# Performance work log

Hardware: AMD Instinct MI355X
Metric: run time of the kernel (lower is better)

The kernel has to match this reference:

```python
import jax, jax.numpy as jnp
import numpy as np

HEADS = 8
DIM_HEAD = 64
DIM_INNER = HEADS * DIM_HEAD  # 512
LLM_EMB = 4096
OUT_DIM = 512
ROPE_BASE = 10000.0
EPS = 1e-6


def rms_norm(x, w):
    # GemmaRMSNorm: normalize in fp32, scale by (1 + weight)
    x32 = x.astype(jnp.float32)
    var = jnp.mean(x32 * x32, axis=-1, keepdims=True)
    out = x32 * jax.lax.rsqrt(var + EPS)
    return (out * (1.0 + w)).astype(x.dtype)


def rope(x, offset):
    # x: [b, h, n, d]; half-split (LLaMA-style) rotary embedding
    d = x.shape[-1]
    n = x.shape[-2]
    inv_freq = 1.0 / (ROPE_BASE ** (jnp.arange(0, d, 2, dtype=jnp.float32) / d))
    pos = jnp.arange(n, dtype=jnp.float32) + offset
    freqs = pos[:, None] * inv_freq[None, :]          # [n, d/2]
    cos = jnp.concatenate([jnp.cos(freqs), jnp.cos(freqs)], axis=-1)  # [n, d]
    sin = jnp.concatenate([jnp.sin(freqs), jnp.sin(freqs)], axis=-1)
    x1, x2 = x[..., : d // 2], x[..., d // 2 :]
    rot = jnp.concatenate([-x2, x1], axis=-1)
    return x * cos + rot * sin


def setup_inputs() -> dict:
    key = jax.random.key(0)
    ks = jax.random.split(key, 20)
    b, n_plan, s_vlm = 4, 1024, 512
    s = 0.02
    return {
        "planning_tokens": jax.random.normal(ks[0], (b, n_plan, DIM_INNER), jnp.float32),
        "vlm_keys": jax.random.normal(ks[1], (b, s_vlm, LLM_EMB), jnp.float32),
        "vlm_values": jax.random.normal(ks[2], (b, s_vlm, LLM_EMB), jnp.float32),
        "W_skv": jax.random.normal(ks[3], (LLM_EMB, DIM_INNER), jnp.float32) * s,
        "b_skv": jnp.zeros((DIM_INNER,), jnp.float32),
        "W_qkv": jax.random.normal(ks[4], (DIM_INNER, 3 * DIM_INNER), jnp.float32) * s,
        "b_qkv": jnp.zeros((3 * DIM_INNER,), jnp.float32),
        "W_out": jax.random.normal(ks[5], (DIM_INNER, DIM_INNER), jnp.float32) * s,
        "b_out": jnp.zeros((DIM_INNER,), jnp.float32),
        "W_ff1": jax.random.normal(ks[6], (DIM_INNER, DIM_INNER), jnp.float32) * s,
        "b_ff1": jnp.zeros((DIM_INNER,), jnp.float32),
        "W_ff2": jax.random.normal(ks[7], (DIM_INNER, OUT_DIM), jnp.float32) * s,
        "b_ff2": jnp.zeros((OUT_DIM,), jnp.float32),
        "g_norm1": jnp.zeros((DIM_INNER,), jnp.float32),
        "g_norm2": jnp.zeros((DIM_INNER,), jnp.float32),
    }


def reference(planning_tokens, vlm_keys, vlm_values, W_skv, b_skv, W_qkv, b_qkv,
              W_out, b_out, W_ff1, b_ff1, W_ff2, b_ff2, g_norm1, g_norm2):
    b, n, _ = planning_tokens.shape
    scale = DIM_HEAD ** -0.5

    normed = rms_norm(planning_tokens, g_norm1)
    qkv = normed @ W_qkv + b_qkv                       # [b, n, 3*dim_inner]
    q, k, v = jnp.split(qkv, 3, axis=-1)
    to_heads = lambda t: t.reshape(b, n, HEADS, DIM_HEAD).transpose(0, 2, 1, 3)
    q, k, v = to_heads(q), to_heads(k), to_heads(v)    # [b, h, n, d]

    # no KV cache: q_len == k_len, offsets 0
    q = rope(q, 0)
    k = rope(k, 0)

    state_kv = jnp.concatenate([vlm_keys, vlm_values], axis=1) @ W_skv + b_skv
    state_len = vlm_keys.shape[1]
    sk, sv = state_kv[:, :state_len], state_kv[:, state_len:]
    sh = lambda t: t.reshape(b, state_len, HEADS, DIM_HEAD).transpose(0, 2, 1, 3)
    sk, sv = sh(sk), sh(sv)                            # [b, h, s, d]

    keys = jnp.concatenate([sk, k], axis=2)            # [b, h, s+n, d]
    values = jnp.concatenate([sv, v], axis=2)

    sim = jnp.einsum('bhid,bhjd->bhij', q, keys) * scale  # [b, h, n, s+n]
    k_len = keys.shape[2]
    # tril(ones(n, k_len), diagonal=state_len): j <= i + state_len
    mask = jnp.arange(k_len)[None, :] <= (jnp.arange(n)[:, None] + state_len)
    sim = jnp.where(mask[None, None], sim, -jnp.inf)
    attn = jax.nn.softmax(sim, axis=-1)

    out = jnp.einsum('bhij,bhjd->bhid', attn, values)  # [b, h, n, d]
    out = out.transpose(0, 2, 1, 3).reshape(b, n, DIM_INNER)
    out = out @ W_out + b_out
    all_out = planning_tokens + out

    ffn = rms_norm(all_out, g_norm2) @ W_ff1 + b_ff1
    ffn = jax.nn.gelu(ffn, approximate=False) @ W_ff2 + b_ff2
    return all_out + ffn
```

## Files before the change

kernel.cpp:

```cpp
#include <hip/hip_runtime.h>
#include <math.h>

typedef unsigned short u16;
typedef unsigned short u16x8 __attribute__((ext_vector_type(8)));
typedef __bf16 bf16v8 __attribute__((ext_vector_type(8)));
typedef float f32x4 __attribute__((ext_vector_type(4)));

static __device__ __forceinline__ float b2f(u16 u){ union{unsigned v; float f;} x; x.v=((unsigned)u)<<16; return x.f; }
static __device__ __forceinline__ u16 f2b(float f){ union{float f; unsigned v;} x; x.f=f; unsigned r=x.v+0x7fffu+((x.v>>16)&1u); return (u16)(r>>16); }
static __device__ __forceinline__ f32x4 mfma16(bf16v8 a, bf16v8 b, f32x4 c){
  return __builtin_amdgcn_mfma_f32_16x16x32_bf16(a,b,c,0,0,0);
}
#define GLDS16(g,l) __builtin_amdgcn_global_load_lds((const __attribute__((address_space(1))) unsigned*)(g), (__attribute__((address_space(3))) unsigned*)(l), 16, 0, 0)

__global__ __launch_bounds__(256) void prep_k(
    const float* __restrict__ vk, const float* __restrict__ vv, u16* __restrict__ vkc, u16* __restrict__ vvc,
    const float* __restrict__ Wqkv, const float* __restrict__ Wskv, const float* __restrict__ Wout,
    const float* __restrict__ Wff1, const float* __restrict__ Wff2,
    u16* __restrict__ Tqkv, u16* __restrict__ Tskv, u16* __restrict__ Tout,
    u16* __restrict__ Tff1, u16* __restrict__ Tff2,
    const float* __restrict__ x, const float* __restrict__ g, u16* __restrict__ o){
  __shared__ u16 tile[64][66];
  int blk = blockIdx.x, t = threadIdx.x;
  if (blk < 8192){
    int i = blk*256 + t;
    const float* s; u16* d; int j;
    if (i < 1048576){ s=vk; d=vkc; j=i; } else { s=vv; d=vvc; j=i-1048576; }
    const float* sp = s + (size_t)j*8;
    f32x4 a = *(const f32x4*)sp, b = *(const f32x4*)(sp+4);
    u16x8 ov;
    #pragma unroll
    for (int k=0;k<4;++k){ ov[k]=f2b(a[k]); ov[k+4]=f2b(b[k]); }
    *(u16x8*)(d + (size_t)j*8) = ov;
    return;
  }
  if (blk < 9088){
    int b2 = blk - 8192;
    const float* in; u16* out; int R, C, lb;
    if (b2 < 192){ in=Wqkv; out=Tqkv; R=512;  C=1536; lb=b2; }
    else if (b2 < 704){ in=Wskv; out=Tskv; R=4096; C=512; lb=b2-192; }
    else if (b2 < 768){ in=Wout; out=Tout; R=512; C=512; lb=b2-704; }
    else if (b2 < 832){ in=Wff1; out=Tff1; R=512; C=512; lb=b2-768; }
    else { in=Wff2; out=Tff2; R=512; C=512; lb=b2-832; }
    int ct = C >> 6;
    int bx = lb % ct, by = lb / ct;
    #pragma unroll
    for (int it=0; it<16; ++it){
      int idx = it*256 + t; int r = idx>>6, c = idx&63;
      tile[r][c] = f2b(in[(size_t)(by*64+r)*C + bx*64 + c]);
    }
    __syncthreads();
    #pragma unroll
    for (int it=0; it<16; ++it){
      int idx = it*256 + t; int c = idx>>6, r = idx&63;
      out[(size_t)(bx*64+c)*R + by*64 + r] = tile[r][c];
    }
    return;
  }
  int w = t>>6, l = t&63;
  size_t row = (size_t)(blk-9088)*4 + w;
  const float* xr = x + row*512 + l*8;
  f32x4 a = *(const f32x4*)xr, b = *(const f32x4*)(xr+4);
  float f[8]; float ss = 0.f;
  #pragma unroll
  for (int j=0;j<4;++j){ f[j]=a[j]; f[j+4]=b[j]; }
  #pragma unroll
  for (int j=0;j<8;++j) ss += f[j]*f[j];
  #pragma unroll
  for (int m=1;m<64;m<<=1) ss += __shfl_xor(ss, m, 64);
  float inv = rsqrtf(ss*(1.0f/512.f) + 1e-6f);
  f32x4 ga = *(const f32x4*)(g + l*8), gb = *(const f32x4*)(g + l*8 + 4);
  u16x8 ov;
  #pragma unroll
  for (int j=0;j<4;++j){ ov[j] = f2b(f[j]*inv*(1.f + ga[j])); ov[j+4] = f2b(f[j+4]*inv*(1.f + gb[j])); }
  *(u16x8*)(o + row*512 + l*8) = ov;
}

__global__ __launch_bounds__(256) void rmsn_k(const float* __restrict__ x, const float* __restrict__ g, u16* __restrict__ o){
  int w = threadIdx.x>>6, l = threadIdx.x&63;
  size_t row = (size_t)blockIdx.x*4 + w;
  const float* xr = x + row*512 + l*8;
  f32x4 a = *(const f32x4*)xr, b = *(const f32x4*)(xr+4);
  float f[8]; float ss = 0.f;
  #pragma unroll
  for (int j=0;j<4;++j){ f[j]=a[j]; f[j+4]=b[j]; }
  #pragma unroll
  for (int j=0;j<8;++j) ss += f[j]*f[j];
  #pragma unroll
  for (int m=1;m<64;m<<=1) ss += __shfl_xor(ss, m, 64);
  float inv = rsqrtf(ss*(1.0f/512.f) + 1e-6f);
  f32x4 ga = *(const f32x4*)(g + l*8), gb = *(const f32x4*)(g + l*8 + 4);
  u16x8 ov;
  #pragma unroll
  for (int j=0;j<4;++j){ ov[j] = f2b(f[j]*inv*(1.f + ga[j])); ov[j+4] = f2b(f[j+4]*inv*(1.f + gb[j])); }
  *(u16x8*)(o + row*512 + l*8) = ov;
}

template<int BM, int BN, int EPI, bool CONCAT, int SPLITS>
__global__ __launch_bounds__(256,2) void gemm_k(
  const u16* __restrict__ A, const u16* __restrict__ Avk, const u16* __restrict__ Avv,
  const u16* __restrict__ BT, const float* __restrict__ bias,
  u16* __restrict__ Cb, float* __restrict__ Cf,
  const float* __restrict__ resid, const float* __restrict__ addf,
  int M, int N, int K)
{
  constexpr int BK = 64;
  constexpr int MFR = BM/32, NFR = BN/32;
  __shared__ alignas(16) u16 sm[(BM+BN)*BK];
  u16* As = sm; u16* Bs = sm + BM*BK;
  const int t = threadIdx.x, w = t>>6, l = t&63, grp = l>>4, l16 = l&15;
  const int wr = w>>1, wc = w&1;
  const int m0 = blockIdx.x*BM, n0 = blockIdx.y*BN;
  const int kchunk = K/SPLITS, kbeg = blockIdx.z*kchunk, kend = kbeg + kchunk;

  f32x4 acc[MFR][NFR];
  #pragma unroll
  for (int m=0;m<MFR;++m)
    #pragma unroll
    for (int n=0;n<NFR;++n) acc[m][n] = f32x4{0.f,0.f,0.f,0.f};

  for (int k0 = kbeg; k0 < kend; k0 += BK){
    #pragma unroll
    for (int it=0; it<MFR; ++it){
      int p16 = it*256 + t;
      int row = p16>>3; int offb = (p16&7)<<4;
      int swz = offb ^ ((row&7)<<4);
      const u16* src;
      if (CONCAT){
        int g = m0+row, bb = g>>10, ii = g&1023;
        const u16* base = (ii < 512) ? (Avk + (size_t)(bb*512+ii)*4096)
                                     : (Avv + (size_t)(bb*512+ii-512)*4096);
        src = base + k0 + (swz>>1);
      } else {
        src = A + (size_t)(m0+row)*K + k0 + (swz>>1);
      }
      GLDS16(src, As + (it*256 + w*64)*8);
    }
    #pragma unroll
    for (int it=0; it<NFR; ++it){
      int p16 = it*256 + t;
      int row = p16>>3; int offb = (p16&7)<<4;
      int swz = offb ^ ((row&7)<<4);
      const u16* src = BT + (size_t)(n0+row)*K + k0 + (swz>>1);
      GLDS16(src, Bs + (it*256 + w*64)*8);
    }
    __syncthreads();

    bf16v8 af[MFR][2], bfr[NFR][2];
    #pragma unroll
    for (int kk=0;kk<2;++kk){
      #pragma unroll
      for (int m=0;m<MFR;++m){
        int row = wr*(BM/2) + m*16 + l16;
        int offb = (kk*64 + grp*16) ^ ((row&7)<<4);
        af[m][kk] = *(const bf16v8*)((const char*)As + row*128 + offb);
      }
      #pragma unroll
      for (int n=0;n<NFR;++n){
        int row = wc*(BN/2) + n*16 + l16;
        int offb = (kk*64 + grp*16) ^ ((row&7)<<4);
        bfr[n][kk] = *(const bf16v8*)((const char*)Bs + row*128 + offb);
      }
    }
    #pragma unroll
    for (int kk=0;kk<2;++kk)
      #pragma unroll
      for (int m=0;m<MFR;++m)
        #pragma unroll
        for (int n=0;n<NFR;++n)
          acc[m][n] = mfma16(af[m][kk], bfr[n][kk], acc[m][n]);
    __syncthreads();
  }

  #pragma unroll
  for (int m=0;m<MFR;++m){
    #pragma unroll
    for (int n=0;n<NFR;++n){
      #pragma unroll
      for (int r=0;r<4;++r){
        int row = m0 + wr*(BM/2) + m*16 + grp*4 + r;
        int col = n0 + wc*(BN/2) + n*16 + l16;
        size_t idx = (size_t)row*N + col;
        if (SPLITS > 1){
          Cf[(size_t)blockIdx.z*M*N + idx] = acc[m][n][r];
        } else {
          float v = acc[m][n][r] + bias[col];
          if (EPI == 0){
            Cb[idx] = f2b(v);
          } else if (EPI == 1){
            Cf[idx] = v + resid[idx];
          } else if (EPI == 2){
            v = 0.5f*v*(1.f + erff(v*0.70710678f));
            Cb[idx] = f2b(v);
          } else {
            Cf[idx] = v + addf[idx];
          }
        }
      }
    }
  }
}

template<int SPLITS>
__global__ __launch_bounds__(256) void combine_k(const float* __restrict__ P, const float* __restrict__ bias,
                                                 u16* __restrict__ outb, int n8, int N){
  int i = blockIdx.x*256 + threadIdx.x;
  if (i >= n8) return;
  size_t base = (size_t)i*8;
  const size_t MN = (size_t)n8*8;
  float acc[8];
  {
    f32x4 a = *(const f32x4*)(P + base), b = *(const f32x4*)(P + base + 4);
    #pragma unroll
    for (int j=0;j<4;++j){ acc[j]=a[j]; acc[j+4]=b[j]; }
  }
  #pragma unroll
  for (int s=1;s<SPLITS;++s){
    f32x4 a = *(const f32x4*)(P + s*MN + base), b = *(const f32x4*)(P + s*MN + base + 4);
    #pragma unroll
    for (int j=0;j<4;++j){ acc[j]+=a[j]; acc[j+4]+=b[j]; }
  }
  int col0 = (int)(base % N);
  u16x8 o;
  #pragma unroll
  for (int j=0;j<8;++j) o[j] = f2b(acc[j] + bias[col0+j]);
  *(u16x8*)(outb + base) = o;
}

__global__ __launch_bounds__(256) void scatter_qk(const u16* __restrict__ qkv, const u16* __restrict__ skv,
                                                  u16* __restrict__ Qh, u16* __restrict__ KEYS){
  int bi = blockIdx.x;
  int b = bi>>10, i = bi&1023;
  int t = threadIdx.x;
  int h = t>>5, dp = t&31;
  const u16* qrow = qkv + (size_t)bi*1536;
  float invf = __expf(-(float)dp * (9.2103403720f/32.f));
  float fr = (float)i * invf;
  float sn, cs; __sincosf(fr, &sn, &cs);
  int bh = b*8 + h;
  float x1 = b2f(qrow[h*64+dp]), x2 = b2f(qrow[h*64+dp+32]);
  u16* qd = Qh + ((size_t)bh*1024 + i)*64;
  qd[dp]    = f2b((x1*cs - x2*sn)*0.125f);
  qd[dp+32] = f2b((x2*cs + x1*sn)*0.125f);
  x1 = b2f(qrow[512+h*64+dp]); x2 = b2f(qrow[512+h*64+dp+32]);
  u16* kd = KEYS + ((size_t)bh*1536 + 512 + i)*64;
  kd[dp]    = f2b(x1*cs - x2*sn);
  kd[dp+32] = f2b(x2*cs + x1*sn);
  if (i < 512){
    const u16* skrow = skv + ((size_t)b*1024 + i)*512;
    for (int e = t; e < 512; e += 256){
      int hh = e>>6, d = e&63;
      KEYS[((size_t)(b*8+hh)*1536 + i)*64 + d] = skrow[e];
    }
  }
}

__global__ __launch_bounds__(256) void build_vt(const u16* __restrict__ qkv, const u16* __restrict__ skv,
                                                u16* __restrict__ VT){
  __shared__ u16 tile[64][66];
  int blk = blockIdx.x;
  int bh = blk / 24, tt = blk % 24;
  int b = bh>>3, h = bh&7;
  int t = threadIdx.x;
  int jbase;
  if (tt < 16){
    int i0 = tt*64; jbase = 512 + i0;
    #pragma unroll
    for (int it=0; it<16; ++it){
      int idx = it*256+t; int r = idx>>6, c = idx&63;
      tile[r][c] = qkv[((size_t)b*1024 + i0 + r)*1536 + 1024 + h*64 + c];
    }
  } else {
    int j0 = (tt-16)*64; jbase = j0;
    #pragma unroll
    for (int it=0; it<16; ++it){
      int idx = it*256+t; int r = idx>>6, c = idx&63;
      tile[r][c] = skv[((size_t)b*1024 + 512 + j0 + r)*512 + h*64 + c];
    }
  }
  __syncthreads();
  #pragma unroll
  for (int it=0; it<16; ++it){
    int idx = it*256+t; int c = idx>>6, r = idx&63;
    VT[((size_t)bh*64 + c)*1536 + jbase + r] = tile[r][c];
  }
}

__global__ __launch_bounds__(256,2) void attn_k(const u16* __restrict__ Qh, const u16* __restrict__ KEYS,
                                                const u16* __restrict__ VT,
                                                float* __restrict__ Op, float2* __restrict__ Ml2){
  __shared__ alignas(16) u16 Ks[2][64*64];
  __shared__ alignas(16) u16 Vs[2][64*64];
  __shared__ alignas(16) u16 Pl[4][2][16*64];
  const int t = threadIdx.x, w = t>>6, l = t&63, grp = l>>4, l16 = l&15;
  const int blk = blockIdx.x;
  const int s = blk & 1, qg = (blk>>1) & 7, bh = blk>>4;
  const int i0 = qg*128 + w*32;
  const int klo = s*768;
  int khi = qg*128 + 640; { int cap = klo + 768; if (khi > cap) khi = cap; }
  const size_t prow = ((size_t)s*32 + bh)*1024;

  if (khi <= klo){
    if (l < 32) Ml2[prow + i0 + l] = make_float2(-1e30f, 0.f);
    return;
  }
  const int nt = (khi - klo) >> 6;

  const u16* Qb = Qh + (size_t)bh*65536;
  const u16* Kb = KEYS + (size_t)bh*98304;
  const u16* Vb = VT + (size_t)bh*98304;
  const int swz = (l16&7)<<4;

  bf16v8 qf[2][2];
  #pragma unroll
  for (int m=0;m<2;++m)
    #pragma unroll
    for (int kk=0;kk<2;++kk)
      qf[m][kk] = *(const bf16v8*)(Qb + (size_t)(i0 + m*16 + l16)*64 + kk*32 + grp*8);

  f32x4 Ot[2][4];
  #pragma unroll
  for (int m=0;m<2;++m)
    #pragma unroll
    for (int n=0;n<4;++n) Ot[m][n] = f32x4{0.f,0.f,0.f,0.f};
  float mrun[2] = {-1e30f,-1e30f}, lrun[2] = {0.f,0.f};

  #pragma unroll
  for (int it=0; it<2; ++it){
    int p16 = it*256 + t; int row = p16>>3; int sb = ((p16&7)<<4) ^ ((row&7)<<4);
    GLDS16(Kb + (size_t)(klo+row)*64 + (sb>>1), &Ks[0][0] + (it*256 + w*64)*8);
    GLDS16(Vb + (size_t)row*1536 + klo + (sb>>1), &Vs[0][0] + (it*256 + w*64)*8);
  }
  __syncthreads();

  for (int tt = 0; tt < nt; ++tt){
    const int j0 = klo + tt*64;
    if (tt+1 < nt){
      const int j1 = j0 + 64, c1 = (tt+1)&1;
      #pragma unroll
      for (int it=0; it<2; ++it){
        int p16 = it*256 + t; int row = p16>>3; int sb = ((p16&7)<<4) ^ ((row&7)<<4);
        GLDS16(Kb + (size_t)(j1+row)*64 + (sb>>1), &Ks[c1][0] + (it*256 + w*64)*8);
        GLDS16(Vb + (size_t)row*1536 + j1 + (sb>>1), &Vs[c1][0] + (it*256 + w*64)*8);
      }
    }
    const int c = tt&1;
    const char* Kt = (const char*)&Ks[c][0];
    const char* Vt = (const char*)&Vs[c][0];

    f32x4 St[2][4];
    #pragma unroll
    for (int m=0;m<2;++m)
      #pragma unroll
      for (int n=0;n<4;++n) St[m][n] = f32x4{0.f,0.f,0.f,0.f};
    #pragma unroll
    for (int kk=0;kk<2;++kk)
      #pragma unroll
      for (int n=0;n<4;++n){
        int row = n*16 + l16;
        bf16v8 kf = *(const bf16v8*)(Kt + row*128 + ((kk*64 + grp*16) ^ swz));
        St[0][n] = mfma16(kf, qf[0][kk], St[0][n]);
        St[1][n] = mfma16(kf, qf[1][kk], St[1][n]);
      }

    #pragma unroll
    for (int m=0;m<2;++m){
      const int qb = i0 + m*16;
      const bool tail = (j0 + 63 > qb + 512);
      const int qlim = qb + l16 + 512;
      float sv[4][4]; float m_loc = -1e30f;
      #pragma unroll
      for (int n=0;n<4;++n)
        #pragma unroll
        for (int r=0;r<4;++r){
          float x = St[m][n][r];
          if (tail && (j0 + n*16 + grp*4 + r > qlim)) x = -1e30f;
          sv[n][r] = x; m_loc = fmaxf(m_loc, x);
        }
      m_loc = fmaxf(m_loc, __shfl_xor(m_loc, 16, 64));
      m_loc = fmaxf(m_loc, __shfl_xor(m_loc, 32, 64));
      float mnew = fmaxf(mrun[m], m_loc);
      float alpha = __expf(mrun[m] - mnew);
      float rs = 0.f;
      unsigned pk[8];
      #pragma unroll
      for (int n=0;n<4;++n)
        #pragma unroll
        for (int c2=0;c2<2;++c2){
          float p0 = __expf(sv[n][2*c2]   - mnew);
          float p1 = __expf(sv[n][2*c2+1] - mnew);
          rs += p0 + p1;
          pk[n*2+c2] = (unsigned)f2b(p0) | ((unsigned)f2b(p1) << 16);
        }
      rs += __shfl_xor(rs, 16, 64);
      rs += __shfl_xor(rs, 32, 64);
      lrun[m] = lrun[m]*alpha + rs;
      mrun[m] = mnew;
      #pragma unroll
      for (int n=0;n<4;++n)
        #pragma unroll
        for (int r=0;r<4;++r) Ot[m][n][r] *= alpha;
      u16* Pw = &Pl[w][m][0];
      #pragma unroll
      for (int n=0;n<4;++n)
        #pragma unroll
        for (int c2=0;c2<2;++c2)
          *(unsigned*)((char*)Pw + l16*128 + ((n*32 + grp*8 + c2*4) ^ swz)) = pk[n*2+c2];
    }

    bf16v8 pb[2][2];
    #pragma unroll
    for (int m=0;m<2;++m){
      const char* Pw = (const char*)&Pl[w][m][0];
      pb[m][0] = *(const bf16v8*)(Pw + l16*128 + ((grp*16)      ^ swz));
      pb[m][1] = *(const bf16v8*)(Pw + l16*128 + ((64 + grp*16) ^ swz));
    }
    #pragma unroll
    for (int n=0;n<4;++n){
      int row = n*16 + l16;
      bf16v8 vf0 = *(const bf16v8*)(Vt + row*128 + ((grp*16)      ^ swz));
      bf16v8 vf1 = *(const bf16v8*)(Vt + row*128 + ((64 + grp*16) ^ swz));
      #pragma unroll
      for (int m=0;m<2;++m){
        Ot[m][n] = mfma16(vf0, pb[m][0], Ot[m][n]);
        Ot[m][n] = mfma16(vf1, pb[m][1], Ot[m][n]);
      }
    }
    __syncthreads();
  }

  #pragma unroll
  for (int m=0;m<2;++m){
    float* Tw = (float*)&Pl[w][m][0];
    #pragma unroll
    for (int hf=0; hf<2; ++hf){
      #pragma unroll
      for (int nn=0; nn<2; ++nn)
        #pragma unroll
        for (int r=0; r<4; ++r)
          *(float*)((char*)Tw + l16*128 + ((((nn*16 + grp*4 + r)*4)) ^ swz)) = Ot[m][hf*2+nn][r];
      f32x4 v0 = *(const f32x4*)((const char*)Tw + l16*128 + ((grp*32)      ^ swz));
      f32x4 v1 = *(const f32x4*)((const char*)Tw + l16*128 + ((grp*32 + 16) ^ swz));
      float* dst = Op + (prow + i0 + m*16 + l16)*64 + hf*32 + grp*8;
      *(f32x4*)dst = v0;
      *(f32x4*)(dst+4) = v1;
    }
  }
  if (grp == 0){
    #pragma unroll
    for (int m=0;m<2;++m)
      Ml2[prow + i0 + m*16 + l16] = make_float2(mrun[m], lrun[m]);
  }
}

__global__ __launch_bounds__(512) void attn_combine(const float* __restrict__ Op, const float2* __restrict__ Ml2,
                                                    u16* __restrict__ AO){
  int bi = blockIdx.x;
  int b = bi>>10, i = bi&1023;
  int t = threadIdx.x; int h = t>>6, d = t&63;
  int bh = b*8 + h;
  float2 ml0 = Ml2[(size_t)bh*1024 + i];
  float2 ml1 = Ml2[((size_t)32 + bh)*1024 + i];
  float M = fmaxf(ml0.x, ml1.x);
  float a0 = (ml0.y > 0.f) ? __expf(ml0.x - M) : 0.f;
  float a1 = (ml1.y > 0.f) ? __expf(ml1.x - M) : 0.f;
  float denom = a0*ml0.y + a1*ml1.y;
  float o = 0.f;
  if (a0 > 0.f) o += a0 * Op[((size_t)bh*1024 + i)*64 + d];
  if (a1 > 0.f) o += a1 * Op[(((size_t)32 + bh)*1024 + i)*64 + d];
  AO[((size_t)b*1024 + i)*512 + h*64 + d] = f2b(o / denom);
}

extern "C" void kernel_launch(void* const* d_in, const int* in_sizes, int n_in,
                              void* d_out, int out_size, void* d_ws, size_t ws_size,
                              hipStream_t stream) {
  const float* planning = (const float*)d_in[0];
  const float* vk   = (const float*)d_in[1];
  const float* vv   = (const float*)d_in[2];
  const float* Wskv = (const float*)d_in[3];
  const float* bskv = (const float*)d_in[4];
  const float* Wqkv = (const float*)d_in[5];
  const float* bqkv = (const float*)d_in[6];
  const float* Wout = (const float*)d_in[7];
  const float* bout = (const float*)d_in[8];
  const float* Wff1 = (const float*)d_in[9];
  const float* bff1 = (const float*)d_in[10];
  const float* Wff2 = (const float*)d_in[11];
  const float* bff2 = (const float*)d_in[12];
  const float* g1   = (const float*)d_in[13];
  const float* g2   = (const float*)d_in[14];
  float* outp = (float*)d_out;

  char* w8 = (char*)d_ws;
  size_t off = 0;
  auto take = [&](size_t n)->char*{ char* p = w8 + off; off += (n + 255) & ~(size_t)255; return p; };
  u16* vkc     = (u16*)take((size_t)4*512*4096*2);
  u16* vvc     = (u16*)take((size_t)4*512*4096*2);
  u16* WTqkv   = (u16*)take((size_t)1536*512*2);
  u16* WTskv   = (u16*)take((size_t)512*4096*2);
  u16* WTout   = (u16*)take((size_t)512*512*2);
  u16* WTff1   = (u16*)take((size_t)512*512*2);
  u16* WTff2   = (u16*)take((size_t)512*512*2);
  u16* normed1 = (u16*)take((size_t)4096*512*2);
  u16* qkv     = (u16*)take((size_t)4096*1536*2);
  u16* skv     = (u16*)take((size_t)4096*512*2);
  u16* Qh      = (u16*)take((size_t)32*1024*64*2);
  u16* KEYS    = (u16*)take((size_t)32*1536*64*2);
  u16* VT      = (u16*)take((size_t)32*64*1536*2);
  u16* AO      = (u16*)take((size_t)4096*512*2);
  float* all_out = (float*)take((size_t)4096*512*4);
  u16* normed2 = (u16*)take((size_t)4096*512*2);
  u16* h1      = (u16*)take((size_t)4096*512*2);
  float* Op    = (float*)take((size_t)2*32*1024*64*4);
  float2* Ml2  = (float2*)take((size_t)2*32*1024*8);
  float* Pd    = (float*)take((size_t)4*4096*512*4);
  (void)in_sizes; (void)n_in; (void)out_size; (void)ws_size;

  prep_k<<<dim3(10112), 256, 0, stream>>>(vk, vv, vkc, vvc,
                                          Wqkv, Wskv, Wout, Wff1, Wff2,
                                          WTqkv, WTskv, WTout, WTff1, WTff2,
                                          planning, g1, normed1);

  gemm_k<64,128,0,false,1><<<dim3(64,12), 256, 0, stream>>>(normed1,nullptr,nullptr, WTqkv, bqkv, qkv, nullptr, nullptr, nullptr, 4096, 1536, 512);
  gemm_k<128,64,0,true, 4><<<dim3(32,8,4), 256, 0, stream>>>(nullptr, vkc, vvc,     WTskv, bskv, nullptr, Pd, nullptr, nullptr, 4096, 512, 4096);
  combine_k<4><<<dim3(1024), 256, 0, stream>>>(Pd, bskv, skv, 262144, 512);

  scatter_qk<<<dim3(4096), 256, 0, stream>>>(qkv, skv, Qh, KEYS);
  build_vt<<<dim3(768), 256, 0, stream>>>(qkv, skv, VT);

  attn_k<<<dim3(512), 256, 0, stream>>>(Qh, KEYS, VT, Op, Ml2);
  attn_combine<<<dim3(4096), 512, 0, stream>>>(Op, Ml2, AO);

  gemm_k<64,64,1,false,1><<<dim3(64,8), 256, 0, stream>>>(AO, nullptr,nullptr, WTout, bout, nullptr, all_out, planning, nullptr, 4096, 512, 512);
  rmsn_k<<<dim3(1024), 256, 0, stream>>>(all_out, g2, normed2);
  gemm_k<64,64,2,false,1><<<dim3(64,8), 256, 0, stream>>>(normed2, nullptr,nullptr, WTff1, bff1, h1, nullptr, nullptr, nullptr, 4096, 512, 512);
  gemm_k<64,64,3,false,1><<<dim3(64,8), 256, 0, stream>>>(h1, nullptr,nullptr, WTff2, bff2, nullptr, outp, nullptr, all_out, 4096, 512, 512);
}
```

Measured before the change: 154.6 us.

## Interleave key tiles across split-K halves and shrink attention query tile

The attention kernel now gives each block 64 query rows (16 per wave) instead of 128, and launches twice as many blocks. Each block works on one of two interleaved halves of the key tiles (even or odd 64-column tiles) rather than a contiguous range. This balances causal-masked work evenly between the two splits and removes the blocks that previously had no work. The cost is that each loaded K/V tile now feeds only 16 query rows per wave, so operand reuse is halved and total K/V traffic goes up.

```diff
diff --git a/kernel.cpp b/kernel.cpp
--- a/kernel.cpp
+++ b/kernel.cpp
@@ -291,166 +291,133 @@
                                                 float* __restrict__ Op, float2* __restrict__ Ml2){
   __shared__ alignas(16) u16 Ks[2][64*64];
   __shared__ alignas(16) u16 Vs[2][64*64];
-  __shared__ alignas(16) u16 Pl[4][2][16*64];
+  __shared__ alignas(16) u16 Pl[4][16*64];
   const int t = threadIdx.x, w = t>>6, l = t&63, grp = l>>4, l16 = l&15;
   const int blk = blockIdx.x;
-  const int s = blk & 1, qg = (blk>>1) & 7, bh = blk>>4;
-  const int i0 = qg*128 + w*32;
-  const int klo = s*768;
-  int khi = qg*128 + 640; { int cap = klo + 768; if (khi > cap) khi = cap; }
+  const int s = blk & 1, qg = (blk>>1) & 15, bh = blk>>5;
+  const int i0 = qg*64 + w*16;
+  int khi = qg*64 + 576; if (khi > 1536) khi = 1536;
+  const int ntt = khi >> 6;
   const size_t prow = ((size_t)s*32 + bh)*1024;
-
-  if (khi <= klo){
-    if (l < 32) Ml2[prow + i0 + l] = make_float2(-1e30f, 0.f);
-    return;
-  }
-  const int nt = (khi - klo) >> 6;
 
   const u16* Qb = Qh + (size_t)bh*65536;
   const u16* Kb = KEYS + (size_t)bh*98304;
   const u16* Vb = VT + (size_t)bh*98304;
+  u16* Pw = &Pl[w][0];
   const int swz = (l16&7)<<4;
-
-  bf16v8 qf[2][2];
-  #pragma unroll
-  for (int m=0;m<2;++m)
-    #pragma unroll
-    for (int kk=0;kk<2;++kk)
-      qf[m][kk] = *(const bf16v8*)(Qb + (size_t)(i0 + m*16 + l16)*64 + kk*32 + grp*8);
-
-  f32x4 Ot[2][4];
-  #pragma unroll
-  for (int m=0;m<2;++m)
-    #pragma unroll
-    for (int n=0;n<4;++n) Ot[m][n] = f32x4{0.f,0.f,0.f,0.f};
-  float mrun[2] = {-1e30f,-1e30f}, lrun[2] = {0.f,0.f};
+  const int qlim = i0 + l16 + 512;
+
+  bf16v8 qf[2];
+  #pragma unroll
+  for (int kk=0;kk<2;++kk)
+    qf[kk] = *(const bf16v8*)(Qb + (size_t)(i0 + l16)*64 + kk*32 + grp*8);
+
+  f32x4 Ot[4];
+  #pragma unroll
+  for (int n=0;n<4;++n) Ot[n] = f32x4{0.f,0.f,0.f,0.f};
+  float mrun = -1e30f, lrun = 0.f;
 
   #pragma unroll
   for (int it=0; it<2; ++it){
     int p16 = it*256 + t; int row = p16>>3; int sb = ((p16&7)<<4) ^ ((row&7)<<4);
-    GLDS16(Kb + (size_t)(klo+row)*64 + (sb>>1), &Ks[0][0] + (it*256 + w*64)*8);
-    GLDS16(Vb + (size_t)row*1536 + klo + (sb>>1), &Vs[0][0] + (it*256 + w*64)*8);
+    GLDS16(Kb + (size_t)(s*64+row)*64 + (sb>>1), &Ks[0][0] + (it*256 + w*64)*8);
+    GLDS16(Vb + (size_t)row*1536 + s*64 + (sb>>1), &Vs[0][0] + (it*256 + w*64)*8);
   }
   __syncthreads();
 
-  for (int tt = 0; tt < nt; ++tt){
-    const int j0 = klo + tt*64;
-    if (tt+1 < nt){
-      const int j1 = j0 + 64, c1 = (tt+1)&1;
+  int buf = 0;
+  for (int tt = s; tt < ntt; tt += 2){
+    const int j0 = tt*64;
+    if (tt+2 < ntt){
+      const int j1 = j0 + 128, nb = buf^1;
       #pragma unroll
       for (int it=0; it<2; ++it){
         int p16 = it*256 + t; int row = p16>>3; int sb = ((p16&7)<<4) ^ ((row&7)<<4);
-        GLDS16(Kb + (size_t)(j1+row)*64 + (sb>>1), &Ks[c1][0] + (it*256 + w*64)*8);
-        GLDS16(Vb + (size_t)row*1536 + j1 + (sb>>1), &Vs[c1][0] + (it*256 + w*64)*8);
-      }
-    }
-    const int c = tt&1;
-    const char* Kt = (const char*)&Ks[c][0];
-    const char* Vt = (const char*)&Vs[c][0];
-
-    f32x4 St[2][4];
-    #pragma unroll
-    for (int m=0;m<2;++m)
-      #pragma unroll
-      for (int n=0;n<4;++n) St[m][n] = f32x4{0.f,0.f,0.f,0.f};
+        GLDS16(Kb + (size_t)(j1+row)*64 + (sb>>1), &Ks[nb][0] + (it*256 + w*64)*8);
+        GLDS16(Vb + (size_t)row*1536 + j1 + (sb>>1), &Vs[nb][0] + (it*256 + w*64)*8);
+      }
+    }
+    const char* Kt = (const char*)&Ks[buf][0];
+    const char* Vt = (const char*)&Vs[buf][0];
+
+    f32x4 St[4];
+    #pragma unroll
+    for (int n=0;n<4;++n) St[n] = f32x4{0.f,0.f,0.f,0.f};
     #pragma unroll
     for (int kk=0;kk<2;++kk)
       #pragma unroll
       for (int n=0;n<4;++n){
         int row = n*16 + l16;
         bf16v8 kf = *(const bf16v8*)(Kt + row*128 + ((kk*64 + grp*16) ^ swz));
-        St[0][n] = mfma16(kf, qf[0][kk], St[0][n]);
-        St[1][n] = mfma16(kf, qf[1][kk], St[1][n]);
-      }
-
-    #pragma unroll
-    for (int m=0;m<2;++m){
-      const int qb = i0 + m*16;
-      const bool tail = (j0 + 63 > qb + 512);
-      const int qlim = qb + l16 + 512;
-      float sv[4][4]; float m_loc = -1e30f;
-      #pragma unroll
-      for (int n=0;n<4;++n)
-        #pragma unroll
-        for (int r=0;r<4;++r){
-          float x = St[m][n][r];
-          if (tail && (j0 + n*16 + grp*4 + r > qlim)) x = -1e30f;
-          sv[n][r] = x; m_loc = fmaxf(m_loc, x);
-        }
-      m_loc = fmaxf(m_loc, __shfl_xor(m_loc, 16, 64));
-      m_loc = fmaxf(m_loc, __shfl_xor(m_loc, 32, 64));
-      float mnew = fmaxf(mrun[m], m_loc);
-      float alpha = __expf(mrun[m] - mnew);
-      float rs = 0.f;
-      unsigned pk[8];
-      #pragma unroll
-      for (int n=0;n<4;++n)
-        #pragma unroll
-        for (int c2=0;c2<2;++c2){
-          float p0 = __expf(sv[n][2*c2]   - mnew);
-          float p1 = __expf(sv[n][2*c2+1] - mnew);
-          rs += p0 + p1;
-          pk[n*2+c2] = (unsigned)f2b(p0) | ((unsigned)f2b(p1) << 16);
-        }
-      rs += __shfl_xor(rs, 16, 64);
-      rs += __shfl_xor(rs, 32, 64);
-      lrun[m] = lrun[m]*alpha + rs;
-      mrun[m] = mnew;
-      #pragma unroll
-      for (int n=0;n<4;++n)
-        #pragma unroll
-        for (int r=0;r<4;++r) Ot[m][n][r] *= alpha;
-      u16* Pw = &Pl[w][m][0];
-      #pragma unroll
-      for (int n=0;n<4;++n)
-        #pragma unroll
-        for (int c2=0;c2<2;++c2)
-          *(unsigned*)((char*)Pw + l16*128 + ((n*32 + grp*8 + c2*4) ^ swz)) = pk[n*2+c2];
-    }
-
-    bf16v8 pb[2][2];
-    #pragma unroll
-    for (int m=0;m<2;++m){
-      const char* Pw = (const char*)&Pl[w][m][0];
-      pb[m][0] = *(const bf16v8*)(Pw + l16*128 + ((grp*16)      ^ swz));
-      pb[m][1] = *(const bf16v8*)(Pw + l16*128 + ((64 + grp*16) ^ swz));
-    }
+        St[n] = mfma16(kf, qf[kk], St[n]);
+      }
+    const bool tail = (j0 + 63 > i0 + 512);
+    float sv[4][4]; float m_loc = -1e30f;
+    #pragma unroll
+    for (int n=0;n<4;++n)
+      #pragma unroll
+      for (int r=0;r<4;++r){
+        float x = St[n][r];
+        if (tail && (j0 + n*16 + grp*4 + r > qlim)) x = -1e30f;
+        sv[n][r] = x; m_loc = fmaxf(m_loc, x);
+      }
+    m_loc = fmaxf(m_loc, __shfl_xor(m_loc, 16, 64));
+    m_loc = fmaxf(m_loc, __shfl_xor(m_loc, 32, 64));
+    float mnew = fmaxf(mrun, m_loc);
+    float alpha = __expf(mrun - mnew);
+    float rs = 0.f;
+    unsigned pk[8];
+    #pragma unroll
+    for (int n=0;n<4;++n)
+      #pragma unroll
+      for (int c2=0;c2<2;++c2){
+        float p0 = __expf(sv[n][2*c2]   - mnew);
+        float p1 = __expf(sv[n][2*c2+1] - mnew);
+        rs += p0 + p1;
+        pk[n*2+c2] = (unsigned)f2b(p0) | ((unsigned)f2b(p1) << 16);
+      }
+    rs += __shfl_xor(rs, 16, 64);
+    rs += __shfl_xor(rs, 32, 64);
+    lrun = lrun*alpha + rs;
+    mrun = mnew;
+    #pragma unroll
+    for (int n=0;n<4;++n)
+      #pragma unroll
+      for (int r=0;r<4;++r) Ot[n][r] *= alpha;
+    #pragma unroll
+    for (int n=0;n<4;++n)
+      #pragma unroll
+      for (int c2=0;c2<2;++c2)
+        *(unsigned*)((char*)Pw + l16*128 + ((n*32 + grp*8 + c2*4) ^ swz)) = pk[n*2+c2];
+    bf16v8 pb0 = *(const bf16v8*)((const char*)Pw + l16*128 + ((grp*16)      ^ swz));
+    bf16v8 pb1 = *(const bf16v8*)((const char*)Pw + l16*128 + ((64 + grp*16) ^ swz));
     #pragma unroll
     for (int n=0;n<4;++n){
       int row = n*16 + l16;
       bf16v8 vf0 = *(const bf16v8*)(Vt + row*128 + ((grp*16)      ^ swz));
       bf16v8 vf1 = *(const bf16v8*)(Vt + row*128 + ((64 + grp*16) ^ swz));
-      #pragma unroll
-      for (int m=0;m<2;++m){
-        Ot[m][n] = mfma16(vf0, pb[m][0], Ot[m][n]);
-        Ot[m][n] = mfma16(vf1, pb[m][1], Ot[m][n]);
-      }
+      Ot[n] = mfma16(vf0, pb0, Ot[n]);
+      Ot[n] = mfma16(vf1, pb1, Ot[n]);
     }
     __syncthreads();
-  }
-
-  #pragma unroll
-  for (int m=0;m<2;++m){
-    float* Tw = (float*)&Pl[w][m][0];
-    #pragma unroll
-    for (int hf=0; hf<2; ++hf){
-      #pragma unroll
-      for (int nn=0; nn<2; ++nn)
-        #pragma unroll
-        for (int r=0; r<4; ++r)
-          *(float*)((char*)Tw + l16*128 + ((((nn*16 + grp*4 + r)*4)) ^ swz)) = Ot[m][hf*2+nn][r];
-      f32x4 v0 = *(const f32x4*)((const char*)Tw + l16*128 + ((grp*32)      ^ swz));
-      f32x4 v1 = *(const f32x4*)((const char*)Tw + l16*128 + ((grp*32 + 16) ^ swz));
-      float* dst = Op + (prow + i0 + m*16 + l16)*64 + hf*32 + grp*8;
-      *(f32x4*)dst = v0;
-      *(f32x4*)(dst+4) = v1;
-    }
-  }
-  if (grp == 0){
-    #pragma unroll
-    for (int m=0;m<2;++m)
-      Ml2[prow + i0 + m*16 + l16] = make_float2(mrun[m], lrun[m]);
-  }
+    buf ^= 1;
+  }
+
+  float* Tw = (float*)Pw;
+  #pragma unroll
+  for (int hf=0; hf<2; ++hf){
+    #pragma unroll
+    for (int nn=0; nn<2; ++nn)
+      #pragma unroll
+      for (int r=0; r<4; ++r)
+        *(float*)((char*)Tw + l16*128 + ((((nn*16 + grp*4 + r)*4)) ^ swz)) = Ot[hf*2+nn][r];
+    f32x4 v0 = *(const f32x4*)((const char*)Tw + l16*128 + ((grp*32)      ^ swz));
+    f32x4 v1 = *(const f32x4*)((const char*)Tw + l16*128 + ((grp*32 + 16) ^ swz));
+    float* dst = Op + (prow + i0 + l16)*64 + hf*32 + grp*8;
+    *(f32x4*)dst = v0;
+    *(f32x4*)(dst+4) = v1;
+  }
+  if (grp == 0) Ml2[prow + i0 + l16] = make_float2(mrun, lrun);
 }
 
 __global__ __launch_bounds__(512) void attn_combine(const float* __restrict__ Op, const float2* __restrict__ Ml2,
@@ -528,7 +495,7 @@
   scatter_qk<<<dim3(4096), 256, 0, stream>>>(qkv, skv, Qh, KEYS);
   build_vt<<<dim3(768), 256, 0, stream>>>(qkv, skv, VT);
 
-  attn_k<<<dim3(512), 256, 0, stream>>>(Qh, KEYS, VT, Op, Ml2);
+  attn_k<<<dim3(1024), 256, 0, stream>>>(Qh, KEYS, VT, Op, Ml2);
   attn_combine<<<dim3(4096), 512, 0, stream>>>(Op, Ml2, AO);
 
   gemm_k<64,64,1,false,1><<<dim3(64,8), 256, 0, stream>>>(AO, nullptr,nullptr, WTout, bout, nullptr, all_out, planning, nullptr, 4096, 512, 512);
```

Measured after the change: 153.1 us. Within noise of the previous version (-0.9%).
